# Performance work log

Hardware: AMD Instinct MI355X
Metric: run time of the kernel (lower is better)

Reference implementation:

```python
import jax, jax.numpy as jnp
import numpy as np

N_HEADS = 16
D_MODEL = 1024
D_K = D_MODEL // N_HEADS


def setup_inputs() -> dict:
    key = jax.random.key(0)
    ks = jax.random.split(key, 7)
    B, S = 2, 2048
    init = 0.02
    return {
        "query": jax.random.normal(ks[0], (B, S, D_MODEL), dtype=jnp.float32),
        "key": jax.random.normal(ks[1], (B, S, D_MODEL), dtype=jnp.float32),
        "value": jax.random.normal(ks[2], (B, S, D_MODEL), dtype=jnp.float32),
        "W_q": jax.random.normal(ks[3], (D_MODEL, D_MODEL), dtype=jnp.float32) * init,
        "W_k": jax.random.normal(ks[4], (D_MODEL, D_MODEL), dtype=jnp.float32) * init,
        "W_v": jax.random.normal(ks[5], (D_MODEL, D_MODEL), dtype=jnp.float32) * init,
        "W_o": jax.random.normal(ks[6], (D_MODEL, D_MODEL), dtype=jnp.float32) * init,
    }


def _split_heads(x):
    # (B, S, d_model) -> (B, H, S, d_k)
    B, S, _ = x.shape
    return x.reshape(B, S, N_HEADS, D_K).transpose(0, 2, 1, 3)


def reference(query, key, value, W_q, W_k, W_v, W_o):
    scale = jnp.sqrt(jnp.asarray(D_K, dtype=query.dtype))
    # torch Linear: y = x @ W.T
    Q = _split_heads(query @ W_q.T)   # (B,H,Sq,dk)
    K = _split_heads(key @ W_k.T)     # (B,H,Sk,dk)
    V = _split_heads(value @ W_v.T)   # (B,H,Sk,dk)
    scores = jnp.einsum("bhqd,bhkd->bhqk", Q, K) / scale
    attn = jax.nn.softmax(scores, axis=-1)           # (B,H,Sq,Sk); dropout p=0 -> identity
    attn_weights = attn.mean(axis=1)                 # (B,Sq,Sk) interpretable weights
    head_out = jnp.einsum("bhqk,bhkd->bqhd", attn, V)  # (B,Sq,H,dk)
    # NOTE: the original computes a head-gating (W_h) whose result is overwritten
    # by the concat below -> dead code, omitted.
    B, Sq = head_out.shape[0], head_out.shape[1]
    out = head_out.reshape(B, Sq, D_MODEL) @ W_o.T   # (B,Sq,d_model)
    return (out, attn_weights)
```

## Files before the change

### kernel.cpp

```cpp
#include <hip/hip_runtime.h>
#include <hip/hip_bf16.h>

#define Bq 2
#define Hh 16
#define Ss 2048
#define Dm 1024
#define Dk 64
#define SCALE 0.125f

typedef _Float16 f16x8 __attribute__((ext_vector_type(8)));
typedef _Float16 f16x4 __attribute__((ext_vector_type(4)));
typedef float    f32x4 __attribute__((ext_vector_type(4)));


__device__ __forceinline__ void gl_lds16(const void* g, void* lds) {
    __builtin_amdgcn_global_load_lds(
        (const __attribute__((address_space(1))) void*)g,
        (__attribute__((address_space(3))) void*)lds, 16, 0, 0);
}

__global__ __launch_bounds__(256) void convert_kernel(
    const float* __restrict__ q, const float* __restrict__ k,
    const float* __restrict__ v, const float* __restrict__ wq,
    const float* __restrict__ wk, const float* __restrict__ wv,
    const float* __restrict__ wo,
    _Float16* __restrict__ qd, _Float16* __restrict__ kd,
    _Float16* __restrict__ vd, _Float16* __restrict__ wd)
{
    int seg = blockIdx.y;
    const float* src; _Float16* dst; int n4;
    switch (seg) {
        case 0: src = q; dst = qd; n4 = 1048576; break;
        case 1: src = k; dst = kd; n4 = 1048576; break;
        case 2: src = v; dst = vd; n4 = 1048576; break;
        default:
            src = (seg == 3) ? wq : (seg == 4) ? wk : (seg == 5) ? wv : wo;
            dst = wd + (size_t)(seg - 3) * 1048576;
            n4 = 262144;
    }
    for (int i = blockIdx.x * 256 + threadIdx.x; i < n4; i += gridDim.x * 256) {
        float4 x = ((const float4*)src)[i];
        f16x4 h = {(_Float16)x.x, (_Float16)x.y, (_Float16)x.z, (_Float16)x.w};
        ((f16x4*)dst)[i] = h;
    }
}

__global__ __launch_bounds__(256) void gemm_qkv(
    const _Float16* __restrict__ qf, const _Float16* __restrict__ kf,
    const _Float16* __restrict__ vf, const _Float16* __restrict__ Wh,
    _Float16* __restrict__ Qd, _Float16* __restrict__ Kd,
    _Float16* __restrict__ Vd)
{
    __shared__ _Float16 As[128 * 32];
    __shared__ _Float16 Ws[128 * 32];
    int z = blockIdx.z;
    const _Float16* A = (z == 0) ? qf : (z == 1) ? kf : vf;
    const _Float16* W = Wh + (size_t)z * (Dm * Dm);
    int t = threadIdx.x, lane = t & 63, w = t >> 6;
    int quad = lane >> 4, l15 = lane & 15;
    int wm = w & 1, wn = w >> 1;
    int n0 = blockIdx.x * 128, m0 = blockIdx.y * 128;

    f32x4 acc[4][4] = {};
    for (int k0 = 0; k0 < Dm; k0 += 32) {
        __syncthreads();
        for (int j = 0; j < 2; ++j) {
            int ca = w * 128 + j * 64 + lane;
            int row = ca >> 2, c8 = (ca & 3) * 8;
            gl_lds16(&A[(size_t)(m0 + row) * Dm + k0 + c8],
                     &As[(size_t)(w * 128 + j * 64) * 8]);
            gl_lds16(&W[(size_t)(n0 + row) * Dm + k0 + c8],
                     &Ws[(size_t)(w * 128 + j * 64) * 8]);
        }
        __syncthreads();
        f16x8 af[4], bf[4];
        for (int mi = 0; mi < 4; ++mi)
            af[mi] = *(const f16x8*)&As[(wm * 64 + mi * 16 + l15) * 32 + quad * 8];
        for (int ni = 0; ni < 4; ++ni)
            bf[ni] = *(const f16x8*)&Ws[(wn * 64 + ni * 16 + l15) * 32 + quad * 8];
        for (int mi = 0; mi < 4; ++mi)
            for (int ni = 0; ni < 4; ++ni)
                acc[mi][ni] = __builtin_amdgcn_mfma_f32_16x16x32_f16(
                    af[mi], bf[ni], acc[mi][ni], 0, 0, 0);
    }
    _Float16* Y = (z == 0) ? Qd : (z == 1) ? Kd : Vd;
    for (int mi = 0; mi < 4; ++mi)
        for (int ni = 0; ni < 4; ++ni)
            for (int r = 0; r < 4; ++r) {
                int m = m0 + wm * 64 + mi * 16 + quad * 4 + r;
                int n = n0 + wn * 64 + ni * 16 + l15;
                int b = m >> 11, s = m & (Ss - 1);
                int h = n >> 6,  d = n & 63;
                _Float16 v = (_Float16)acc[mi][ni][r];
                if (z < 2)
                    Y[(((size_t)(b * Hh + h) * Ss + s) << 6) + d] = v;
                else
                    Y[((size_t)(b * Hh + h) * Dk + d) * Ss + s] = v;
            }
}

__global__ __launch_bounds__(256) void gemm_out(
    const _Float16* __restrict__ HO, const _Float16* __restrict__ Woh,
    float* __restrict__ out)
{
    __shared__ _Float16 As[128 * 32];
    __shared__ _Float16 Ws[64 * 32];
    int t = threadIdx.x, lane = t & 63, w = t >> 6;
    int quad = lane >> 4, l15 = lane & 15;
    int n0 = blockIdx.x * 64, m0 = blockIdx.y * 128;

    f32x4 acc[2][4] = {};
    for (int k0 = 0; k0 < Dm; k0 += 32) {
        __syncthreads();
        for (int j = 0; j < 2; ++j) {
            int ca = w * 128 + j * 64 + lane;
            int row = ca >> 2, c8 = (ca & 3) * 8;
            gl_lds16(&HO[(size_t)(m0 + row) * Dm + k0 + c8],
                     &As[(size_t)(w * 128 + j * 64) * 8]);
        }
        {
            int cw = w * 64 + lane;
            int row = cw >> 2, c8 = (cw & 3) * 8;
            gl_lds16(&Woh[(size_t)(n0 + row) * Dm + k0 + c8],
                     &Ws[(size_t)(w * 64) * 8]);
        }
        __syncthreads();
        f16x8 af[2], bf[4];
        for (int mi = 0; mi < 2; ++mi)
            af[mi] = *(const f16x8*)&As[(w * 32 + mi * 16 + l15) * 32 + quad * 8];
        for (int ni = 0; ni < 4; ++ni)
            bf[ni] = *(const f16x8*)&Ws[(ni * 16 + l15) * 32 + quad * 8];
        for (int mi = 0; mi < 2; ++mi)
            for (int ni = 0; ni < 4; ++ni)
                acc[mi][ni] = __builtin_amdgcn_mfma_f32_16x16x32_f16(
                    af[mi], bf[ni], acc[mi][ni], 0, 0, 0);
    }
    for (int mi = 0; mi < 2; ++mi)
        for (int ni = 0; ni < 4; ++ni)
            for (int r = 0; r < 4; ++r) {
                int m = m0 + w * 32 + mi * 16 + quad * 4 + r;
                int n = n0 + ni * 16 + l15;
                out[(size_t)m * Dm + n] = acc[mi][ni][r];
            }
}

__global__ __launch_bounds__(256) void flash_kernel(
    const _Float16* __restrict__ Qh, const _Float16* __restrict__ Kh,
    const _Float16* __restrict__ Vt, _Float16* __restrict__ Op,
    float* __restrict__ lp)
{
    __shared__ alignas(16) _Float16 Ks[64][72];
    __shared__ alignas(16) _Float16 Vs[64][72];
    __shared__ alignas(16) _Float16 Ps[4][32][72];
    int t = threadIdx.x;
    int lane = t & 63, w = t >> 6;
    int quad = lane >> 4, l15 = lane & 15;
    int bh = blockIdx.x;
    int q0 = blockIdx.y * 128 + w * 32;
    int ks = blockIdx.z;
    int kt0 = ks * 16, kt1 = kt0 + 16;

    const _Float16* Qp = Qh + (size_t)bh * Ss * Dk;
    const _Float16* Kp = Kh + (size_t)bh * Ss * Dk;
    const _Float16* Vp = Vt + (size_t)bh * Dk * Ss;

    f16x8 qf[2][2];
    for (int qh = 0; qh < 2; ++qh)
        for (int kf = 0; kf < 2; ++kf)
            qf[qh][kf] = *(const f16x8*)
                &Qp[(size_t)(q0 + qh * 16 + l15) * Dk + kf * 32 + quad * 8];

    int row0 = t >> 3,         col0 = (t & 7) * 8;
    int row1 = (256 + t) >> 3, col1 = col0;

    f16x8 kr0 = *(const f16x8*)&Kp[(size_t)(kt0 * 64 + row0) * Dk + col0];
    f16x8 kr1 = *(const f16x8*)&Kp[(size_t)(kt0 * 64 + row1) * Dk + col1];
    f16x8 vr0 = *(const f16x8*)&Vp[(size_t)row0 * Ss + kt0 * 64 + col0];
    f16x8 vr1 = *(const f16x8*)&Vp[(size_t)row1 * Ss + kt0 * 64 + col1];

    f32x4 o_acc[2][4] = {};
    float lsum[2] = {0.f, 0.f};

    for (int kt = kt0; kt < kt1; ++kt) {
        __syncthreads();
        *(f16x8*)&Ks[row0][col0] = kr0;
        *(f16x8*)&Ks[row1][col1] = kr1;
        *(f16x8*)&Vs[row0][col0] = vr0;
        *(f16x8*)&Vs[row1][col1] = vr1;
        if (kt + 1 < kt1) {
            kr0 = *(const f16x8*)&Kp[(size_t)((kt + 1) * 64 + row0) * Dk + col0];
            kr1 = *(const f16x8*)&Kp[(size_t)((kt + 1) * 64 + row1) * Dk + col1];
            vr0 = *(const f16x8*)&Vp[(size_t)row0 * Ss + (kt + 1) * 64 + col0];
            vr1 = *(const f16x8*)&Vp[(size_t)row1 * Ss + (kt + 1) * 64 + col1];
        }
        __syncthreads();

        for (int nt = 0; nt < 4; ++nt) {
            f16x8 kf0 = *(const f16x8*)&Ks[nt * 16 + l15][quad * 8];
            f16x8 kf1 = *(const f16x8*)&Ks[nt * 16 + l15][32 + quad * 8];
            for (int qh = 0; qh < 2; ++qh) {
                f32x4 z = {};
                z = __builtin_amdgcn_mfma_f32_16x16x32_f16(kf0, qf[qh][0], z, 0, 0, 0);
                z = __builtin_amdgcn_mfma_f32_16x16x32_f16(kf1, qf[qh][1], z, 0, 0, 0);
                float p0 = __expf(z[0] * SCALE);
                float p1 = __expf(z[1] * SCALE);
                float p2 = __expf(z[2] * SCALE);
                float p3 = __expf(z[3] * SCALE);
                lsum[qh] += (p0 + p1) + (p2 + p3);
                f16x4 hv = {(_Float16)p0, (_Float16)p1, (_Float16)p2, (_Float16)p3};
                *(f16x4*)&Ps[w][qh * 16 + l15][nt * 16 + quad * 4] = hv;
            }
        }

        f16x8 vf[4][2];
        for (int dt = 0; dt < 4; ++dt) {
            vf[dt][0] = *(const f16x8*)&Vs[dt * 16 + l15][quad * 8];
            vf[dt][1] = *(const f16x8*)&Vs[dt * 16 + l15][32 + quad * 8];
        }
        for (int qh = 0; qh < 2; ++qh) {
            f16x8 pf0 = *(const f16x8*)&Ps[w][qh * 16 + l15][quad * 8];
            f16x8 pf1 = *(const f16x8*)&Ps[w][qh * 16 + l15][32 + quad * 8];
            for (int dt = 0; dt < 4; ++dt) {
                o_acc[qh][dt] = __builtin_amdgcn_mfma_f32_16x16x32_f16(
                    pf0, vf[dt][0], o_acc[qh][dt], 0, 0, 0);
                o_acc[qh][dt] = __builtin_amdgcn_mfma_f32_16x16x32_f16(
                    pf1, vf[dt][1], o_acc[qh][dt], 0, 0, 0);
            }
        }
    }

    for (int qh = 0; qh < 2; ++qh) {
        lsum[qh] += __shfl_xor(lsum[qh], 16);
        lsum[qh] += __shfl_xor(lsum[qh], 32);
    }

    _Float16* Od = Op + (size_t)ks * (Bq * Hh * Ss * Dk) + (size_t)bh * Ss * Dk;
    for (int qh = 0; qh < 2; ++qh) {
        for (int dt = 0; dt < 4; ++dt)
            for (int r = 0; r < 4; ++r) {
                int q = q0 + qh * 16 + quad * 4 + r;
                Od[(size_t)q * Dk + dt * 16 + l15] = (_Float16)o_acc[qh][dt][r];
            }
        if (lane < 16)
            lp[(size_t)ks * 65536 + (size_t)bh * Ss + q0 + qh * 16 + lane] = lsum[qh];
    }
}

__global__ __launch_bounds__(256) void reduce_kernel(
    const _Float16* __restrict__ Op, const float* __restrict__ lp,
    _Float16* __restrict__ HO, float* __restrict__ lw)
{
    int i = blockIdx.x * 256 + threadIdx.x;
    int d4  = i & 15;
    int row = i >> 4;
    f16x4 a = ((const f16x4*)Op)[i];
    f16x4 b = ((const f16x4*)Op)[i + 1048576];
    float l = lp[row] + lp[65536 + row];
    float inv = 1.0f / l;
    int bh = row >> 11, q = row & (Ss - 1);
    int b_ = bh >> 4,  h = bh & 15;
    f16x4 o;
    for (int j = 0; j < 4; ++j)
        o[j] = (_Float16)(((float)a[j] + (float)b[j]) * inv);
    *(f16x4*)&HO[((size_t)(b_ * Ss + q)) * Dm + h * Dk + d4 * 4] = o;
    if (d4 == 0) lw[row] = l;
}

__global__ __launch_bounds__(256) void attn_mean_kernel(
    const _Float16* __restrict__ Qh, const _Float16* __restrict__ Kh,
    const float* __restrict__ lw, float* __restrict__ out_attn)
{
    __shared__ alignas(16) _Float16 Ks[64][72];
    int t = threadIdx.x;
    int lane = t & 63, w = t >> 6;
    int quad = lane >> 4, l15 = lane & 15;
    int k0 = blockIdx.x * 64;
    int q0 = blockIdx.y * 128;
    int b  = blockIdx.z;
    int qrow = q0 + w * 32;

    int srow0 = t >> 3, scol0 = (t & 7) * 8;
    int srow1 = (256 + t) >> 3, scol1 = scol0;

    f16x8 kr0, kr1, qn[2][2];
    float4 ln[2];
    {
        size_t base = (size_t)(b * Hh) * Ss;
        kr0 = *(const f16x8*)&Kh[(base + k0 + srow0) * Dk + scol0];
        kr1 = *(const f16x8*)&Kh[(base + k0 + srow1) * Dk + scol1];
        for (int qh = 0; qh < 2; ++qh) {
            qn[qh][0] = *(const f16x8*)&Qh[(base + qrow + qh * 16 + l15) * Dk + quad * 8];
            qn[qh][1] = *(const f16x8*)&Qh[(base + qrow + qh * 16 + l15) * Dk + 32 + quad * 8];
            ln[qh] = *(const float4*)&lw[base + qrow + qh * 16 + quad * 4];
        }
    }

    f32x4 acc[2][4] = {};
    for (int h = 0; h < Hh; ++h) {
        __syncthreads();
        *(f16x8*)&Ks[srow0][scol0] = kr0;
        *(f16x8*)&Ks[srow1][scol1] = kr1;
        f16x8 qf[2][2];
        float4 lv[2];
        for (int qh = 0; qh < 2; ++qh) {
            qf[qh][0] = qn[qh][0]; qf[qh][1] = qn[qh][1]; lv[qh] = ln[qh];
        }
        if (h < Hh - 1) {
            size_t base = (size_t)(b * Hh + h + 1) * Ss;
            kr0 = *(const f16x8*)&Kh[(base + k0 + srow0) * Dk + scol0];
            kr1 = *(const f16x8*)&Kh[(base + k0 + srow1) * Dk + scol1];
            for (int qh = 0; qh < 2; ++qh) {
                qn[qh][0] = *(const f16x8*)&Qh[(base + qrow + qh * 16 + l15) * Dk + quad * 8];
                qn[qh][1] = *(const f16x8*)&Qh[(base + qrow + qh * 16 + l15) * Dk + 32 + quad * 8];
                ln[qh] = *(const float4*)&lw[base + qrow + qh * 16 + quad * 4];
            }
        }
        __syncthreads();

        float ir[2][4];
        for (int qh = 0; qh < 2; ++qh) {
            ir[qh][0] = 1.0f / lv[qh].x; ir[qh][1] = 1.0f / lv[qh].y;
            ir[qh][2] = 1.0f / lv[qh].z; ir[qh][3] = 1.0f / lv[qh].w;
        }
        for (int nt = 0; nt < 4; ++nt) {
            f16x8 b0 = *(const f16x8*)&Ks[nt * 16 + l15][quad * 8];
            f16x8 b1 = *(const f16x8*)&Ks[nt * 16 + l15][32 + quad * 8];
            for (int qh = 0; qh < 2; ++qh) {
                f32x4 z = {};
                z = __builtin_amdgcn_mfma_f32_16x16x32_f16(qf[qh][0], b0, z, 0, 0, 0);
                z = __builtin_amdgcn_mfma_f32_16x16x32_f16(qf[qh][1], b1, z, 0, 0, 0);
                for (int r = 0; r < 4; ++r)
                    acc[qh][nt][r] += __expf(z[r] * SCALE) * ir[qh][r];
            }
        }
    }

    for (int qh = 0; qh < 2; ++qh)
        for (int nt = 0; nt < 4; ++nt)
            for (int r = 0; r < 4; ++r) {
                int q = qrow + qh * 16 + quad * 4 + r;
                out_attn[((size_t)(b * Ss + q)) * Ss + k0 + nt * 16 + l15] =
                    acc[qh][nt][r] * (1.0f / Hh);
            }
}

extern "C" void kernel_launch(void* const* d_in, const int* in_sizes, int n_in,
                              void* d_out, int out_size, void* d_ws, size_t ws_size,
                              hipStream_t stream) {
    const float* query = (const float*)d_in[0];
    const float* key   = (const float*)d_in[1];
    const float* value = (const float*)d_in[2];
    const float* Wq    = (const float*)d_in[3];
    const float* Wk    = (const float*)d_in[4];
    const float* Wv    = (const float*)d_in[5];
    const float* Wo    = (const float*)d_in[6];

    float* out      = (float*)d_out;
    float* attn_out = out + (size_t)4194304;

    _Float16* HO  = (_Float16*)attn_out;
    _Float16* qf  = (_Float16*)(attn_out + 2097152);
    _Float16* kf  = qf + 4194304;
    _Float16* vf  = kf + 4194304;
    _Float16* Op  = qf;
    float*    lp  = (float*)(Op + 2 * 4194304);

    _Float16* Qh = (_Float16*)d_ws;
    _Float16* Kh = Qh + (size_t)4194304;
    _Float16* Vt = Kh + (size_t)4194304;
    _Float16* Wh = Vt + (size_t)4194304;
    float*    lw = (float*)(Wh + (size_t)4194304);

    convert_kernel<<<dim3(256, 7), 256, 0, stream>>>(
        query, key, value, Wq, Wk, Wv, Wo, qf, kf, vf, Wh);

    gemm_qkv<<<dim3(8, 32, 3), 256, 0, stream>>>(qf, kf, vf, Wh, Qh, Kh, Vt);

    flash_kernel<<<dim3(Bq * Hh, Ss / 128, 2), 256, 0, stream>>>(Qh, Kh, Vt, Op, lp);

    reduce_kernel<<<4096, 256, 0, stream>>>(Op, lp, HO, lw);

    gemm_out<<<dim3(16, 32), 256, 0, stream>>>(HO, Wh + (size_t)3 * 1048576, out);

    attn_mean_kernel<<<dim3(Ss / 64, Ss / 128, Bq), 256, 0, stream>>>(
        Qh, Kh, lw, attn_out);
}
```

Baseline: 290.6 us.

## Fold softmax scale into Q projection, use exp2 and compute row sums via MFMA

The softmax scale and the log2(e) factor are folded into the Q projection epilogue, so both attention kernels can call a raw hardware exp2 without a per-element multiply. In the flash kernel, the row sums of P move from per-lane scalar adds plus cross-lane shuffles to an extra MFMA against a vector of ones. Divisions become fast reciprocals, and packed fp16 conversion is used. The row sum is now taken from fp16-rounded probabilities, and the reciprocal is slightly less accurate.

After: 273.9 us. 1.06x faster.

```diff
diff --git a/kernel.cpp b/kernel.cpp
--- a/kernel.cpp
+++ b/kernel.cpp
@@ -6,10 +6,11 @@
 #define Ss 2048
 #define Dm 1024
 #define Dk 64
-#define SCALE 0.125f
+#define QSC 0.18033688f
 
 typedef _Float16 f16x8 __attribute__((ext_vector_type(8)));
 typedef _Float16 f16x4 __attribute__((ext_vector_type(4)));
+typedef _Float16 f16x2 __attribute__((ext_vector_type(2)));
 typedef float    f32x4 __attribute__((ext_vector_type(4)));
 
 
@@ -17,6 +18,28 @@
     __builtin_amdgcn_global_load_lds(
         (const __attribute__((address_space(1))) void*)g,
         (__attribute__((address_space(3))) void*)lds, 16, 0, 0);
+}
+
+extern "C" __device__ float __ocml_exp2_f32(float);
+
+__device__ __forceinline__ float exp2_fast(float x) {
+#if __has_builtin(__builtin_amdgcn_exp2f)
+    return __builtin_amdgcn_exp2f(x);
+#else
+    return __ocml_exp2_f32(x);
+#endif
+}
+
+__device__ __forceinline__ float rcp_fast(float x) {
+#if __has_builtin(__builtin_amdgcn_rcpf)
+    return __builtin_amdgcn_rcpf(x);
+#else
+    float r; asm("v_rcp_f32 %0, %1" : "=v"(r) : "v"(x)); return r;
+#endif
+}
+
+__device__ __forceinline__ f16x2 pk_f16(float a, float b) {
+    return __builtin_bit_cast(f16x2, __builtin_amdgcn_cvt_pkrtz(a, b));
 }
 
 __global__ __launch_bounds__(256) void convert_kernel(
@@ -84,6 +107,7 @@
                     af[mi], bf[ni], acc[mi][ni], 0, 0, 0);
     }
     _Float16* Y = (z == 0) ? Qd : (z == 1) ? Kd : Vd;
+    float osc = (z == 0) ? QSC : 1.0f;
     for (int mi = 0; mi < 4; ++mi)
         for (int ni = 0; ni < 4; ++ni)
             for (int r = 0; r < 4; ++r) {
@@ -91,7 +115,7 @@
                 int n = n0 + wn * 64 + ni * 16 + l15;
                 int b = m >> 11, s = m & (Ss - 1);
                 int h = n >> 6,  d = n & 63;
-                _Float16 v = (_Float16)acc[mi][ni][r];
+                _Float16 v = (_Float16)(acc[mi][ni][r] * osc);
                 if (z < 2)
                     Y[(((size_t)(b * Hh + h) * Ss + s) << 6) + d] = v;
                 else
@@ -170,6 +194,9 @@
             qf[qh][kf] = *(const f16x8*)
                 &Qp[(size_t)(q0 + qh * 16 + l15) * Dk + kf * 32 + quad * 8];
 
+    const _Float16 one = (_Float16)1.0f;
+    const f16x8 ones = {one, one, one, one, one, one, one, one};
+
     int row0 = t >> 3,         col0 = (t & 7) * 8;
     int row1 = (256 + t) >> 3, col1 = col0;
 
@@ -179,7 +206,7 @@
     f16x8 vr1 = *(const f16x8*)&Vp[(size_t)row1 * Ss + kt0 * 64 + col1];
 
     f32x4 o_acc[2][4] = {};
-    float lsum[2] = {0.f, 0.f};
+    f32x4 l_acc[2] = {};
 
     for (int kt = kt0; kt < kt1; ++kt) {
         __syncthreads();
@@ -202,12 +229,9 @@
                 f32x4 z = {};
                 z = __builtin_amdgcn_mfma_f32_16x16x32_f16(kf0, qf[qh][0], z, 0, 0, 0);
                 z = __builtin_amdgcn_mfma_f32_16x16x32_f16(kf1, qf[qh][1], z, 0, 0, 0);
-                float p0 = __expf(z[0] * SCALE);
-                float p1 = __expf(z[1] * SCALE);
-                float p2 = __expf(z[2] * SCALE);
-                float p3 = __expf(z[3] * SCALE);
-                lsum[qh] += (p0 + p1) + (p2 + p3);
-                f16x4 hv = {(_Float16)p0, (_Float16)p1, (_Float16)p2, (_Float16)p3};
+                f16x2 h0 = pk_f16(exp2_fast(z[0]), exp2_fast(z[1]));
+                f16x2 h1 = pk_f16(exp2_fast(z[2]), exp2_fast(z[3]));
+                f16x4 hv = {h0[0], h0[1], h1[0], h1[1]};
                 *(f16x4*)&Ps[w][qh * 16 + l15][nt * 16 + quad * 4] = hv;
             }
         }
@@ -220,6 +244,10 @@
         for (int qh = 0; qh < 2; ++qh) {
             f16x8 pf0 = *(const f16x8*)&Ps[w][qh * 16 + l15][quad * 8];
             f16x8 pf1 = *(const f16x8*)&Ps[w][qh * 16 + l15][32 + quad * 8];
+            l_acc[qh] = __builtin_amdgcn_mfma_f32_16x16x32_f16(
+                pf0, ones, l_acc[qh], 0, 0, 0);
+            l_acc[qh] = __builtin_amdgcn_mfma_f32_16x16x32_f16(
+                pf1, ones, l_acc[qh], 0, 0, 0);
             for (int dt = 0; dt < 4; ++dt) {
                 o_acc[qh][dt] = __builtin_amdgcn_mfma_f32_16x16x32_f16(
                     pf0, vf[dt][0], o_acc[qh][dt], 0, 0, 0);
@@ -227,11 +255,6 @@
                     pf1, vf[dt][1], o_acc[qh][dt], 0, 0, 0);
             }
         }
-    }
-
-    for (int qh = 0; qh < 2; ++qh) {
-        lsum[qh] += __shfl_xor(lsum[qh], 16);
-        lsum[qh] += __shfl_xor(lsum[qh], 32);
     }
 
     _Float16* Od = Op + (size_t)ks * (Bq * Hh * Ss * Dk) + (size_t)bh * Ss * Dk;
@@ -241,8 +264,10 @@
                 int q = q0 + qh * 16 + quad * 4 + r;
                 Od[(size_t)q * Dk + dt * 16 + l15] = (_Float16)o_acc[qh][dt][r];
             }
-        if (lane < 16)
-            lp[(size_t)ks * 65536 + (size_t)bh * Ss + q0 + qh * 16 + lane] = lsum[qh];
+        if (l15 == 0)
+            for (int r = 0; r < 4; ++r)
+                lp[(size_t)ks * 65536 + (size_t)bh * Ss + q0 + qh * 16 +
+                   quad * 4 + r] = l_acc[qh][r];
     }
 }
 
@@ -256,7 +281,7 @@
     f16x4 a = ((const f16x4*)Op)[i];
     f16x4 b = ((const f16x4*)Op)[i + 1048576];
     float l = lp[row] + lp[65536 + row];
-    float inv = 1.0f / l;
+    float inv = rcp_fast(l);
     int bh = row >> 11, q = row & (Ss - 1);
     int b_ = bh >> 4,  h = bh & 15;
     f16x4 o;
@@ -319,8 +344,8 @@
 
         float ir[2][4];
         for (int qh = 0; qh < 2; ++qh) {
-            ir[qh][0] = 1.0f / lv[qh].x; ir[qh][1] = 1.0f / lv[qh].y;
-            ir[qh][2] = 1.0f / lv[qh].z; ir[qh][3] = 1.0f / lv[qh].w;
+            ir[qh][0] = rcp_fast(lv[qh].x); ir[qh][1] = rcp_fast(lv[qh].y);
+            ir[qh][2] = rcp_fast(lv[qh].z); ir[qh][3] = rcp_fast(lv[qh].w);
         }
         for (int nt = 0; nt < 4; ++nt) {
             f16x8 b0 = *(const f16x8*)&Ks[nt * 16 + l15][quad * 8];
@@ -330,7 +355,7 @@
                 z = __builtin_amdgcn_mfma_f32_16x16x32_f16(qf[qh][0], b0, z, 0, 0, 0);
                 z = __builtin_amdgcn_mfma_f32_16x16x32_f16(qf[qh][1], b1, z, 0, 0, 0);
                 for (int r = 0; r < 4; ++r)
-                    acc[qh][nt][r] += __expf(z[r] * SCALE) * ir[qh][r];
+                    acc[qh][nt][r] += exp2_fast(z[r]) * ir[qh][r];
             }
         }
     }
```
